# Performance work log

Hardware: AMD Instinct MI355X
Metric: run time of the kernel (lower is better)

Reference implementation:

```python
import jax, jax.numpy as jnp
import numpy as np

B, IN_F, N_HID = 2048, 512, 2048
HEAD = N_HID + IN_F  # 2560


def setup_inputs() -> dict:
    key = jax.random.key(0)
    ks = jax.random.split(key, 14)
    scale = 1.0 / np.sqrt(HEAD)
    # sparsity mask: original [IN_F, N_HID] in {-1,0,1}; _prep_mask pads with
    # ones [N_HID, N_HID], transposes, abs -> [N_HID, HEAD] of {0,1}
    raw = jax.random.randint(ks[0], (IN_F, N_HID), -1, 2).astype(jnp.float32)
    mask = jnp.abs(jnp.concatenate([raw, jnp.ones((N_HID, N_HID), jnp.float32)], axis=0).T)
    def w(k):
        return jax.random.normal(k, (N_HID, HEAD), jnp.float32) * scale
    def b(k):
        return jax.random.normal(k, (N_HID,), jnp.float32) * scale
    return {
        "x": jax.random.normal(ks[1], (B, IN_F), jnp.float32),
        "hidden": jax.random.normal(ks[2], (B, N_HID), jnp.float32),
        "mask": mask,
        "Wg": w(ks[3]), "bg": b(ks[4]),
        "Wh": w(ks[5]), "bh": b(ks[6]),
        "Wfg": w(ks[7]), "bfg": b(ks[8]),
        "Wfh": w(ks[9]), "bfh": b(ks[10]),
        "Wp": w(ks[11]), "bp": b(ks[12]),
    }


def reference(x, hidden, mask, Wg, bg, Wh, bh, Wfg, bfg, Wfh, bfh, Wp, bp):
    # concatenated input shared by all 5 masked linears: [B, HEAD]
    xc = jnp.concatenate([x, hidden], axis=1)
    # fuse the 5 masked GEMMs into one: [5, N_HID, HEAD] stacked weights
    W_all = jnp.stack([Wg, Wh, Wfg, Wfh, Wp]) * mask[None]
    b_all = jnp.stack([bg, bh, bfg, bfh, bp])
    outs = jnp.einsum('bh,koh->kbo', xc, W_all) + b_all[:, None, :]  # [5, B, N_HID]
    g_out, h_out, fg_out, fh_out, p_out = outs
    g = jnp.tanh(g_out)
    h = jnp.tanh(h_out)
    gate = jax.nn.sigmoid(fg_out + fh_out)
    new_hidden = g * (1.0 - gate) + gate * h
    y_pred = p_out + new_hidden
    return (y_pred, new_hidden)
```

## Files before the change

kernel.cpp:

```cpp
#include <hip/hip_runtime.h>

#define MDIM 2048
#define KD   2560
#define NHID 2048
#define INF  512
#define NS   40

typedef __attribute__((ext_vector_type(4))) float f32x4;
typedef __attribute__((ext_vector_type(8))) short short8;
typedef __attribute__((ext_vector_type(8))) unsigned short ushort8v;
typedef __attribute__((ext_vector_type(4))) unsigned short ushort4v;

#define AS1 __attribute__((address_space(1)))
#define AS3 __attribute__((address_space(3)))

__device__ __forceinline__ unsigned short f2bf(float f) {
    unsigned u = __float_as_uint(f);
    u += 0x7fffu + ((u >> 16) & 1u);
    return (unsigned short)(u >> 16);
}

#define XCB 2560
__global__ void prep_all(const float* __restrict__ x, const float* __restrict__ h,
                         unsigned short* __restrict__ xc,
                         const float* __restrict__ Wg, const float* __restrict__ Wh,
                         const float* __restrict__ Wfg, const float* __restrict__ Wfh,
                         const float* __restrict__ Wp, const float* __restrict__ mask,
                         unsigned short* __restrict__ Wm) {
    if (blockIdx.x < XCB) {
        int idx = blockIdx.x * 256 + threadIdx.x;
        int e = idx * 8;
        int b = e / KD;
        int c = e - b * KD;
        const float* src = (c < INF) ? (x + (size_t)b * INF + c)
                                     : (h + (size_t)b * NHID + (c - INF));
        float4 v0 = *(const float4*)src;
        float4 v1 = *(const float4*)(src + 4);
        ushort8v o;
        o[0] = f2bf(v0.x); o[1] = f2bf(v0.y); o[2] = f2bf(v0.z); o[3] = f2bf(v0.w);
        o[4] = f2bf(v1.x); o[5] = f2bf(v1.y); o[6] = f2bf(v1.z); o[7] = f2bf(v1.w);
        *(ushort8v*)(xc + e) = o;
    } else {
        int idx = (blockIdx.x - XCB) * 256 + threadIdx.x;
        size_t e = (size_t)idx * 4;
        const size_t PL = (size_t)NHID * KD;
        int col = (int)(e % KD);
        float4 m;
        if (col < INF) m = *(const float4*)(mask + e);
        else           m = make_float4(1.f, 1.f, 1.f, 1.f);
        const float* Ws[5] = {Wg, Wh, Wfg, Wfh, Wp};
        #pragma unroll
        for (int k = 0; k < 5; ++k) {
            float4 w = *(const float4*)(Ws[k] + e);
            ushort4v o;
            o[0] = f2bf(w.x * m.x); o[1] = f2bf(w.y * m.y);
            o[2] = f2bf(w.z * m.z); o[3] = f2bf(w.w * m.w);
            *(ushort4v*)(Wm + k * PL + e) = o;
        }
    }
}

#define MFMA16(d, va, vb) d = __builtin_amdgcn_mfma_f32_16x16x32_bf16(va, vb, d, 0, 0, 0)

__global__ __launch_bounds__(512, 2) void gemm_fused(
    const unsigned short* __restrict__ A,
    const unsigned short* __restrict__ Bm,
    const float* __restrict__ bg, const float* __restrict__ bh,
    const float* __restrict__ bfg, const float* __restrict__ bfh,
    const float* __restrict__ bp,
    float* __restrict__ out) {
    __shared__ unsigned short lsA[2][256 * 64];
    __shared__ unsigned short lsB[2][320 * 64];

    const int tid  = threadIdx.x;
    const int lane = tid & 63;
    const int w    = tid >> 6;
    const int wm   = w >> 2;
    const int wn   = w & 3;
    const int lr   = lane & 15;
    const int kq   = lane >> 4;
    const int l7   = lane & 7;
    const int m0   = blockIdx.y * 256;
    const int n0c  = blockIdx.x * 64;

    const unsigned short* gA = A + (size_t)m0 * KD;
    const int soff = (lane >> 3) * KD + (((lane & 7) ^ (lane >> 3)) << 3);
    const int ar0 = (w >> 2) * 128 + (w & 3) * 8;
    const int br0 = (w >> 1) * 80 + (w & 1) * 8;

#define SA(j, t, b) __builtin_amdgcn_global_load_lds( \
        (const AS1 unsigned int*)(gA + (size_t)(ar0 + 32 * (j)) * KD + (t) * 64 + soff), \
        (AS3 unsigned int*)(&lsA[b][(ar0 + 32 * (j)) * 64]), 16, 0, 0)
#define SB(j, t, b) do { \
        const int r0_ = br0 + 16 * (j); \
        const int grow_ = (r0_ >> 6) * NHID + n0c + (r0_ & 63); \
        __builtin_amdgcn_global_load_lds( \
            (const AS1 unsigned int*)(Bm + (size_t)grow_ * KD + (t) * 64 + soff), \
            (AS3 unsigned int*)(&lsB[b][r0_ * 64]), 16, 0, 0); \
    } while (0)

    const int c0 = ((0 + kq) ^ l7) << 3;
    const int c1 = ((4 + kq) ^ l7) << 3;
    const int arow = wm * 128 + lr;
    const int browb = wn * 16 + lr;

#define LDA(b, m, cs) (*(const short8*)&lsA[b][(arow + 16 * (m)) * 64 + (cs)])
#define LDB(b, p, cs) (*(const short8*)&lsB[b][((p) * 64 + browb) * 64 + (cs)])

#define BAR() do { __builtin_amdgcn_s_barrier(); \
                   __builtin_amdgcn_sched_barrier(0); } while (0)

    f32x4 acc[8][5] = {};

    SA(0, 0, 0); SA(1, 0, 0); SA(2, 0, 0); SA(3, 0, 0);
    SB(0, 0, 0); SB(1, 0, 0); SB(2, 0, 0); SB(3, 0, 0); SB(4, 0, 0);
    SB(0, 1, 1); SB(1, 1, 1); SB(2, 1, 1); SB(3, 1, 1); SB(4, 1, 1);
    asm volatile("s_waitcnt vmcnt(5)" ::: "memory");
    __builtin_amdgcn_s_barrier();

    for (int kt = 0; kt < NS; ++kt) {
        const int bc = kt & 1, bo = bc ^ 1;
        short8 av[4], bv0[5], bv1[5];

        if (kt < NS - 1) { SA(0, kt + 1, bo); SA(1, kt + 1, bo); }
        __builtin_amdgcn_sched_barrier(0);
        asm volatile("s_waitcnt vmcnt(7)" ::: "memory");
        BAR();
        #pragma unroll
        for (int i = 0; i < 4; ++i) av[i] = LDA(bc, i, c0);
        #pragma unroll
        for (int p = 0; p < 5; ++p) bv0[p] = LDB(bc, p, c0);
        BAR();
        __builtin_amdgcn_s_setprio(1);
        #pragma unroll
        for (int i = 0; i < 4; ++i)
            #pragma unroll
            for (int p = 0; p < 5; ++p) MFMA16(acc[i][p], av[i], bv0[p]);
        __builtin_amdgcn_s_setprio(0);
        BAR();

        #pragma unroll
        for (int i = 0; i < 4; ++i) av[i] = LDA(bc, i, c1);
        #pragma unroll
        for (int p = 0; p < 5; ++p) bv1[p] = LDB(bc, p, c1);
        if (kt < NS - 1) { SA(2, kt + 1, bo); SA(3, kt + 1, bo); }
        BAR();
        __builtin_amdgcn_s_setprio(1);
        #pragma unroll
        for (int i = 0; i < 4; ++i)
            #pragma unroll
            for (int p = 0; p < 5; ++p) MFMA16(acc[i][p], av[i], bv1[p]);
        __builtin_amdgcn_s_setprio(0);
        BAR();

        #pragma unroll
        for (int i = 0; i < 4; ++i) av[i] = LDA(bc, 4 + i, c0);
        if (kt < NS - 2) { SB(0, kt + 2, bc); SB(1, kt + 2, bc); }
        BAR();
        __builtin_amdgcn_s_setprio(1);
        #pragma unroll
        for (int i = 0; i < 4; ++i)
            #pragma unroll
            for (int p = 0; p < 5; ++p) MFMA16(acc[4 + i][p], av[i], bv0[p]);
        __builtin_amdgcn_s_setprio(0);
        BAR();

        #pragma unroll
        for (int i = 0; i < 4; ++i) av[i] = LDA(bc, 4 + i, c1);
        if (kt < NS - 2) { SB(2, kt + 2, bc); SB(3, kt + 2, bc); SB(4, kt + 2, bc); }
        BAR();
        __builtin_amdgcn_s_setprio(1);
        #pragma unroll
        for (int i = 0; i < 4; ++i)
            #pragma unroll
            for (int p = 0; p < 5; ++p) MFMA16(acc[4 + i][p], av[i], bv1[p]);
        __builtin_amdgcn_s_setprio(0);
        BAR();
    }

    const int col = n0c + wn * 16 + lr;
    const float bgv = bg[col];
    const float bhv = bh[col];
    const float bfv = bfg[col] + bfh[col];
    const float bpv = bp[col];
    const size_t PL = (size_t)MDIM * NHID;
    #pragma unroll
    for (int m = 0; m < 8; ++m) {
        #pragma unroll
        for (int j = 0; j < 4; ++j) {
            const int row = m0 + wm * 128 + m * 16 + kq * 4 + j;
            float gx = acc[m][0][j] + bgv;
            float hx = acc[m][1][j] + bhv;
            float sx = acc[m][2][j] + acc[m][3][j] + bfv;
            float tg = __expf(-2.0f * fabsf(gx));
            float g  = __builtin_copysignf((1.0f - tg) / (1.0f + tg), gx);
            float th = __expf(-2.0f * fabsf(hx));
            float hh = __builtin_copysignf((1.0f - th) / (1.0f + th), hx);
            float gate = 1.0f / (1.0f + __expf(-sx));
            float nh = g * (1.0f - gate) + gate * hh;
            float y  = acc[m][4][j] + bpv + nh;
            out[(size_t)row * NHID + col]      = y;
            out[PL + (size_t)row * NHID + col] = nh;
        }
    }
#undef SA
#undef SB
#undef LDA
#undef LDB
#undef BAR
}

extern "C" void kernel_launch(void* const* d_in, const int* in_sizes, int n_in,
                              void* d_out, int out_size, void* d_ws, size_t ws_size,
                              hipStream_t stream) {
    const float* x      = (const float*)d_in[0];
    const float* hidden = (const float*)d_in[1];
    const float* mask   = (const float*)d_in[2];
    const float* Wg     = (const float*)d_in[3];
    const float* bg     = (const float*)d_in[4];
    const float* Wh     = (const float*)d_in[5];
    const float* bh     = (const float*)d_in[6];
    const float* Wfg    = (const float*)d_in[7];
    const float* bfg    = (const float*)d_in[8];
    const float* Wfh    = (const float*)d_in[9];
    const float* bfh    = (const float*)d_in[10];
    const float* Wp     = (const float*)d_in[11];
    const float* bp     = (const float*)d_in[12];
    float* out = (float*)d_out;

    const size_t need = (size_t)MDIM * KD * 2 + (size_t)5 * NHID * KD * 2;
    if (ws_size < need) return;

    unsigned short* xc = (unsigned short*)d_ws;
    unsigned short* Wm = xc + (size_t)MDIM * KD;

    prep_all<<<XCB + NHID * KD / 4 / 256, 256, 0, stream>>>(
        x, hidden, xc, Wg, Wh, Wfg, Wfh, Wp, mask, Wm);
    dim3 grid(NHID / 64, MDIM / 256);
    gemm_fused<<<grid, 512, 0, stream>>>(xc, Wm, bg, bh, bfg, bfh, bp, out);
}
```

Baseline: 141.2 us.

## Simplify GEMM pipeline to single-stage prefetch with full drain per k-step

Replaces the staggered pipeline, where A is prefetched one k-step ahead and B two k-steps ahead with partial vmcnt waits, with a simpler scheme. Both A and B for the next k-step are now issued across the first three MFMA phases, and the loop waits for all loads (vmcnt(0)) plus a barrier at the end of each iteration. This cuts prefetch depth and removes one barrier per phase boundary, which lowers sync overhead. The cost is less latency hiding for global-to-LDS loads, since each iteration must fully drain its outstanding loads before the next one starts.

```diff
diff --git a/kernel.cpp b/kernel.cpp
--- a/kernel.cpp
+++ b/kernel.cpp
@@ -101,81 +101,78 @@
 
     const int c0 = ((0 + kq) ^ l7) << 3;
     const int c1 = ((4 + kq) ^ l7) << 3;
-    const int arow = wm * 128 + lr;
+    const int arow  = wm * 128 + lr;
     const int browb = wn * 16 + lr;
 
 #define LDA(b, m, cs) (*(const short8*)&lsA[b][(arow + 16 * (m)) * 64 + (cs)])
 #define LDB(b, p, cs) (*(const short8*)&lsB[b][((p) * 64 + browb) * 64 + (cs)])
 
-#define BAR() do { __builtin_amdgcn_s_barrier(); \
-                   __builtin_amdgcn_sched_barrier(0); } while (0)
+#define PBAR() do { __builtin_amdgcn_s_barrier(); \
+                    __builtin_amdgcn_sched_barrier(0); } while (0)
 
     f32x4 acc[8][5] = {};
 
     SA(0, 0, 0); SA(1, 0, 0); SA(2, 0, 0); SA(3, 0, 0);
     SB(0, 0, 0); SB(1, 0, 0); SB(2, 0, 0); SB(3, 0, 0); SB(4, 0, 0);
-    SB(0, 1, 1); SB(1, 1, 1); SB(2, 1, 1); SB(3, 1, 1); SB(4, 1, 1);
-    asm volatile("s_waitcnt vmcnt(5)" ::: "memory");
+    asm volatile("s_waitcnt vmcnt(0)" ::: "memory");
     __builtin_amdgcn_s_barrier();
 
     for (int kt = 0; kt < NS; ++kt) {
         const int bc = kt & 1, bo = bc ^ 1;
-        short8 av[4], bv0[5], bv1[5];
-
-        if (kt < NS - 1) { SA(0, kt + 1, bo); SA(1, kt + 1, bo); }
-        __builtin_amdgcn_sched_barrier(0);
-        asm volatile("s_waitcnt vmcnt(7)" ::: "memory");
-        BAR();
-        #pragma unroll
-        for (int i = 0; i < 4; ++i) av[i] = LDA(bc, i, c0);
-        #pragma unroll
-        for (int p = 0; p < 5; ++p) bv0[p] = LDB(bc, p, c0);
-        BAR();
-        __builtin_amdgcn_s_setprio(1);
-        #pragma unroll
-        for (int i = 0; i < 4; ++i)
-            #pragma unroll
-            for (int p = 0; p < 5; ++p) MFMA16(acc[i][p], av[i], bv0[p]);
-        __builtin_amdgcn_s_setprio(0);
-        BAR();
-
-        #pragma unroll
-        for (int i = 0; i < 4; ++i) av[i] = LDA(bc, i, c1);
-        #pragma unroll
-        for (int p = 0; p < 5; ++p) bv1[p] = LDB(bc, p, c1);
-        if (kt < NS - 1) { SA(2, kt + 1, bo); SA(3, kt + 1, bo); }
-        BAR();
-        __builtin_amdgcn_s_setprio(1);
-        #pragma unroll
-        for (int i = 0; i < 4; ++i)
-            #pragma unroll
-            for (int p = 0; p < 5; ++p) MFMA16(acc[i][p], av[i], bv1[p]);
-        __builtin_amdgcn_s_setprio(0);
-        BAR();
-
-        #pragma unroll
-        for (int i = 0; i < 4; ++i) av[i] = LDA(bc, 4 + i, c0);
-        if (kt < NS - 2) { SB(0, kt + 2, bc); SB(1, kt + 2, bc); }
-        BAR();
-        __builtin_amdgcn_s_setprio(1);
-        #pragma unroll
-        for (int i = 0; i < 4; ++i)
-            #pragma unroll
-            for (int p = 0; p < 5; ++p) MFMA16(acc[4 + i][p], av[i], bv0[p]);
-        __builtin_amdgcn_s_setprio(0);
-        BAR();
-
-        #pragma unroll
-        for (int i = 0; i < 4; ++i) av[i] = LDA(bc, 4 + i, c1);
-        if (kt < NS - 2) { SB(2, kt + 2, bc); SB(3, kt + 2, bc); SB(4, kt + 2, bc); }
-        BAR();
-        __builtin_amdgcn_s_setprio(1);
-        #pragma unroll
-        for (int i = 0; i < 4; ++i)
-            #pragma unroll
-            for (int p = 0; p < 5; ++p) MFMA16(acc[4 + i][p], av[i], bv1[p]);
-        __builtin_amdgcn_s_setprio(0);
-        BAR();
+        const bool st = (kt + 1 < NS);
+        short8 aL[4], aH[4], b0[5], b1[5];
+
+        #pragma unroll
+        for (int m = 0; m < 4; ++m) aL[m] = LDA(bc, m, c0);
+        #pragma unroll
+        for (int n = 0; n < 5; ++n) b0[n] = LDB(bc, n, c0);
+        if (st) { SA(0, kt + 1, bo); SA(1, kt + 1, bo); SA(2, kt + 1, bo); }
+        PBAR();
+        __builtin_amdgcn_s_setprio(1);
+        #pragma unroll
+        for (int m = 0; m < 4; ++m)
+            #pragma unroll
+            for (int n = 0; n < 5; ++n) MFMA16(acc[m][n], aL[m], b0[n]);
+        __builtin_amdgcn_s_setprio(0);
+        PBAR();
+
+        #pragma unroll
+        for (int m = 0; m < 4; ++m) aL[m] = LDA(bc, m, c1);
+        #pragma unroll
+        for (int n = 0; n < 5; ++n) b1[n] = LDB(bc, n, c1);
+        if (st) { SA(3, kt + 1, bo); SB(0, kt + 1, bo); SB(1, kt + 1, bo); }
+        PBAR();
+        __builtin_amdgcn_s_setprio(1);
+        #pragma unroll
+        for (int m = 0; m < 4; ++m)
+            #pragma unroll
+            for (int n = 0; n < 5; ++n) MFMA16(acc[m][n], aL[m], b1[n]);
+        __builtin_amdgcn_s_setprio(0);
+        PBAR();
+
+        #pragma unroll
+        for (int m = 0; m < 4; ++m) aH[m] = LDA(bc, 4 + m, c0);
+        if (st) { SB(2, kt + 1, bo); SB(3, kt + 1, bo); SB(4, kt + 1, bo); }
+        PBAR();
+        __builtin_amdgcn_s_setprio(1);
+        #pragma unroll
+        for (int m = 0; m < 4; ++m)
+            #pragma unroll
+            for (int n = 0; n < 5; ++n) MFMA16(acc[4 + m][n], aH[m], b0[n]);
+        __builtin_amdgcn_s_setprio(0);
+        PBAR();
+
+        #pragma unroll
+        for (int m = 0; m < 4; ++m) aH[m] = LDA(bc, 4 + m, c1);
+        PBAR();
+        __builtin_amdgcn_s_setprio(1);
+        #pragma unroll
+        for (int m = 0; m < 4; ++m)
+            #pragma unroll
+            for (int n = 0; n < 5; ++n) MFMA16(acc[4 + m][n], aH[m], b1[n]);
+        __builtin_amdgcn_s_setprio(0);
+        asm volatile("s_waitcnt vmcnt(0)" ::: "memory");
+        __builtin_amdgcn_s_barrier();
     }
 
     const int col = n0c + wn * 16 + lr;
@@ -207,7 +204,7 @@
 #undef SB
 #undef LDA
 #undef LDB
-#undef BAR
+#undef PBAR
 }
 
 extern "C" void kernel_launch(void* const* d_in, const int* in_sizes, int n_in,
```

New measurement: 130.7 us. 1.08x faster.
